# Performance work log

Hardware: AMD Instinct MI355X
Metric: run time of the kernel (lower is better)

## Reference

```python
import jax, jax.numpy as jnp
import numpy as np

K = 8  # leader_num
S = 8  # state_num


def setup_inputs() -> dict:
    key = jax.random.key(0)
    ks = jax.random.split(key, 11)
    B, L, C, H = 16, 720, 128, 96
    F2 = H // 2 + 1
    OUT = F2 * (2 * K + 1)
    return {
        "x": jax.random.normal(ks[0], (B, L, C), jnp.float32),
        "y_hat": jax.random.normal(ks[1], (B, H, C), jnp.float32),
        "temperature": jnp.ones((1,), jnp.float32),
        "cls_w": jax.random.normal(ks[2], (S, L), jnp.float32) * 0.02,
        "basic_state": jax.random.normal(ks[3], (C, S), jnp.float32) * 0.02,
        "state_bias": jax.random.normal(ks[4], (S,), jnp.float32) * 0.02,
        "mix_head_w": jax.random.normal(ks[5], (S, K * OUT), jnp.float32) * 0.05,
        "mix_head_b": jax.random.normal(ks[6], (S, OUT), jnp.float32) * 0.05,
        "mix_wr": jax.random.normal(ks[7], (F2, 3 * F2), jnp.float32) * 0.05,
        "mix_wi": jax.random.normal(ks[8], (F2, 3 * F2), jnp.float32) * 0.05,
        "mix_br": jax.random.normal(ks[9], (F2,), jnp.float32) * 0.05,
        "mix_bi": jax.random.normal(ks[10], (F2,), jnp.float32) * 0.05,
    }


def _leader_pipeline(xn, yn):
    # xn: [B,C,L] instance-normed lookback, yn: [B,C,H] normed forecast
    B, C, L = xn.shape
    H = yn.shape[-1]
    rf = jnp.fft.rfft(xn, axis=-1)  # [B,C,F]
    # full pairwise circular cross-correlation: [B,C,C,L]
    cc = jnp.fft.irfft(rf[:, :, None, :] * jnp.conj(rf)[:, None, :, :], n=L, axis=-1)
    ca = jnp.abs(cc)
    # local-max masking on interior points (drops first/last lag)
    mask = (ca[..., 1:-1] >= ca[..., :-2]) & (ca[..., 1:-1] >= ca[..., 2:])
    cc = cc[..., 1:-1] * mask / L  # [B,C,C,L-2]
    ca = jnp.abs(cc)
    shift = jnp.argmax(ca, axis=-1)  # [B,C,C] best lag per pair
    cmax = jnp.max(ca, axis=-1)
    _, leader_ids = jax.lax.top_k(cmax, K)  # [B,C,K]
    lead_corr = jnp.take_along_axis(cc, leader_ids[:, :, :, None], axis=2)  # [B,C,K,L-2]
    shift = jnp.take_along_axis(shift, leader_ids, axis=2)  # [B,C,K]
    r = jnp.take_along_axis(lead_corr, shift[..., None], axis=3)[..., 0]  # [B,C,K]
    shift = shift + 1  # account for the dropped first lag (local_max=True)
    # gather leader sequences and apply per-(sample,channel,leader) dynamic shift
    const_idx = jnp.arange(L, L + H)
    idx = const_idx[None, None, :] - shift.reshape(B, C * K, 1)  # [B,CK,H]
    seq = jnp.concatenate([xn, yn], -1)  # [B,C,L+H]
    seq = seq[jnp.arange(B)[:, None], leader_ids.reshape(B, C * K)]  # [B,CK,L+H]
    seq_shifted = jnp.take_along_axis(seq, idx, axis=-1).reshape(B, C, K, H)
    seq_shifted = seq_shifted * jnp.sign(r)[..., None]
    return seq_shifted, jnp.abs(r)


def reference(x, y_hat, temperature, cls_w, basic_state, state_bias,
              mix_head_w, mix_head_b, mix_wr, mix_wi, mix_br, mix_bi):
    B, L, C = x.shape
    H = y_hat.shape[1]
    F2 = H // 2 + 1
    xt = jnp.swapaxes(x, 1, 2)  # [B,C,L]
    yt = jnp.swapaxes(y_hat, 1, 2)  # [B,C,H]
    mu = xt.mean(-1, keepdims=True)
    xc = xt - mu
    std = jnp.sqrt((xc ** 2).mean(-1, keepdims=True) + 1e-8)
    xn = xc / std
    yn = (yt - mu) / std
    seq_shifted, r_abs = _leader_pipeline(xn, yn)  # torch.no_grad block
    seq_shifted = jax.lax.stop_gradient(seq_shifted)
    r_abs = jax.lax.stop_gradient(r_abs)
    ones = jnp.ones((B, C, 1), xt.dtype)
    rw = jax.nn.softmax(jnp.concatenate([ones, r_abs], -1) / temperature, axis=-1)
    corr_feat = rw[..., 1:]  # [B,C,K]
    # FilterFactory (num_state > 1, need_classifier): per-sample state mixture
    p = jax.nn.softmax(state_bias + basic_state + jnp.einsum('bcl,sl->bcs', xt, cls_w), axis=-1)  # [B,C,S]
    OUT = F2 * (2 * K + 1)
    w = jnp.einsum('bcs,sf->bcf', p, mix_head_w).reshape(B, C, K, OUT)
    b = jnp.einsum('bcs,so->bco', p, mix_head_b)
    filt = (jnp.einsum('bck,bcko->bco', corr_feat, w) + b).reshape(B, C, 2 * K + 1, F2)
    yf = jnp.fft.rfft(yn, axis=-1)  # [B,C,F2] complex64
    ssf = jnp.fft.rfft(seq_shifted, axis=-1) * filt[:, :, :K]  # [B,C,K,F2]
    sdf = (ssf - yf[:, :, None]) * filt[:, :, K:2 * K]
    yff = yf * filt[:, :, -1]
    catf = jnp.concatenate([ssf.sum(2), sdf.sum(2), yff], -1)  # [B,C,3*F2]
    mix_w = jax.lax.complex(mix_wr, mix_wi)  # [F2, 3*F2]
    mix_b = jax.lax.complex(mix_br, mix_bi)
    out_f = jnp.einsum('bcf,of->bco', catf, mix_w) + mix_b
    yn_new = yn + jnp.fft.irfft(out_f, n=H, axis=-1)
    y = yn_new * std + mu
    return jnp.swapaxes(y, 1, 2)  # [B,H,C]
```

## Files before the change

### kernel.cpp

```cpp
#include <hip/hip_runtime.h>
#include <math.h>

#define B_ 16
#define L_ 720
#define C_ 128
#define H_ 96
#define F2_ 49
#define K_ 8
#define S_ 8
#define OUT_ 833
#define SEQLEN 816
#define NF 361

__device__ __forceinline__ float2 cmulp(float2 a, float2 w) {
  return make_float2(a.x*w.x - a.y*w.y, a.x*w.y + a.y*w.x);
}

#define WSYNC() do { asm volatile("s_waitcnt lgkmcnt(0)" ::: "memory"); __builtin_amdgcn_sched_barrier(0); } while (0)

__device__ __constant__ float W5X[5] = {1.f, 0.30901699437494742f, -0.80901699437494745f, -0.80901699437494745f, 0.30901699437494742f};
__device__ __constant__ float W5Y[5] = {0.f, 0.95105651629515357f, 0.58778525229247312f, -0.58778525229247312f, -0.95105651629515357f};

__device__ __forceinline__ void dft8_pos(const float2 zin[8], float2 X[8]) {
  const float RH = 0.70710678118654752440f;
  const float2 A0 = make_float2(zin[0].x+zin[4].x, zin[0].y+zin[4].y);
  const float2 A1 = make_float2(zin[0].x-zin[4].x, zin[0].y-zin[4].y);
  const float2 A2 = make_float2(zin[2].x+zin[6].x, zin[2].y+zin[6].y);
  const float2 A3 = make_float2(zin[2].x-zin[6].x, zin[2].y-zin[6].y);
  const float2 A4 = make_float2(zin[1].x+zin[5].x, zin[1].y+zin[5].y);
  const float2 A5 = make_float2(zin[1].x-zin[5].x, zin[1].y-zin[5].y);
  const float2 A6 = make_float2(zin[3].x+zin[7].x, zin[3].y+zin[7].y);
  const float2 A7 = make_float2(zin[3].x-zin[7].x, zin[3].y-zin[7].y);
  const float2 B0 = make_float2(A0.x+A2.x, A0.y+A2.y);
  const float2 B1 = make_float2(A0.x-A2.x, A0.y-A2.y);
  const float2 B2 = make_float2(A4.x+A6.x, A4.y+A6.y);
  const float2 B3 = make_float2(A4.x-A6.x, A4.y-A6.y);
  X[0] = make_float2(B0.x+B2.x, B0.y+B2.y);
  X[4] = make_float2(B0.x-B2.x, B0.y-B2.y);
  X[2] = make_float2(B1.x - B3.y, B1.y + B3.x);
  X[6] = make_float2(B1.x + B3.y, B1.y - B3.x);
  const float2 CI   = make_float2(-A3.y, A3.x);
  const float2 W1s1 = make_float2((A5.x - A5.y)*RH, (A5.x + A5.y)*RH);
  const float2 W3s1 = make_float2((-A5.x - A5.y)*RH, (A5.x - A5.y)*RH);
  const float2 W1s3 = make_float2((A7.x - A7.y)*RH, (A7.x + A7.y)*RH);
  const float2 W3s3 = make_float2((-A7.x - A7.y)*RH, (A7.x - A7.y)*RH);
  X[1] = make_float2(A1.x + CI.x + W1s1.x + W3s3.x, A1.y + CI.y + W1s1.y + W3s3.y);
  X[5] = make_float2(A1.x + CI.x - W1s1.x - W3s3.x, A1.y + CI.y - W1s1.y - W3s3.y);
  X[3] = make_float2(A1.x - CI.x + W3s1.x + W1s3.x, A1.y - CI.y + W3s1.y + W1s3.y);
  X[7] = make_float2(A1.x - CI.x - W3s1.x - W1s3.x, A1.y - CI.y - W3s1.y - W1s3.y);
}

__global__ __launch_bounds__(256) void k0_tab(float2* __restrict__ wtab_g) {
  for (int k = threadIdx.x; k < L_; k += 256) {
    double ang = (double)k * 0.008726646259971647884;
    wtab_g[k] = make_float2((float)cos(ang), (float)sin(ang));
  }
}

__global__ __launch_bounds__(256) void k1_norm(const float* __restrict__ x,
                                               const float* __restrict__ yh,
                                               float* __restrict__ seq,
                                               float* __restrict__ mu_g,
                                               float* __restrict__ std_g) {
  const int bc = blockIdx.x;
  const int b = bc >> 7, c = bc & 127;
  const int tid = threadIdx.x;
  __shared__ float redA[4], redB[4];
  const float* xb = x + (size_t)b * L_ * C_ + c;

  float s = 0.f;
  for (int l = tid; l < L_; l += 256) s += xb[(size_t)l * C_];
  for (int off = 32; off; off >>= 1) s += __shfl_down(s, off, 64);
  if ((tid & 63) == 0) redA[tid >> 6] = s;
  __syncthreads();
  const float mu = (redA[0] + redA[1] + redA[2] + redA[3]) * (1.0f / L_);

  float vs = 0.f;
  for (int l = tid; l < L_; l += 256) { float d = xb[(size_t)l * C_] - mu; vs += d * d; }
  for (int off = 32; off; off >>= 1) vs += __shfl_down(vs, off, 64);
  if ((tid & 63) == 0) redB[tid >> 6] = vs;
  __syncthreads();
  const float stdv = sqrtf((redB[0] + redB[1] + redB[2] + redB[3]) * (1.0f / L_) + 1e-8f);
  const float inv = 1.0f / stdv;

  float* sq = seq + (size_t)bc * SEQLEN;
  for (int l = tid; l < L_; l += 256) sq[l] = (xb[(size_t)l * C_] - mu) * inv;
  const float* yb = yh + (size_t)b * H_ * C_ + c;
  for (int h = tid; h < H_; h += 256) sq[L_ + h] = (yb[(size_t)h * C_] - mu) * inv;
  if (tid == 0) { mu_g[bc] = mu; std_g[bc] = stdv; }
}

__global__ __launch_bounds__(256) void k1f_fwd(const float* __restrict__ seq,
                                               const float2* __restrict__ wtab_g,
                                               float2* __restrict__ Rc) {
  const int bc0 = blockIdx.x * 2;
  const int tid = threadIdx.x;
  __shared__ float xrow[2][L_];
  __shared__ float2 wt[L_];
  for (int k = tid; k < L_; k += 256) {
    wt[k] = wtab_g[k];
    xrow[0][k] = seq[(size_t)bc0 * SEQLEN + k];
    xrow[1][k] = seq[(size_t)(bc0 + 1) * SEQLEN + k];
  }
  __syncthreads();
  for (int u = tid; u < 2 * NF; u += 256) {
    const int row = u / NF, f = u - row * NF;
    float re = 0.f, im = 0.f;
    int m = 0;
    const float* xr = xrow[row];
    for (int l = 0; l < L_; ++l) {
      const float v = xr[l];
      const float2 w = wt[m];
      re = fmaf(v, w.x, re);
      im = fmaf(-v, w.y, im);
      m += f; if (m >= L_) m -= L_;
    }
    Rc[(size_t)(bc0 + row) * NF + f] = make_float2(re, im);
  }
}

__global__ __launch_bounds__(256, 2) void k2_fft(const float2* __restrict__ Rc,
                                                 const float2* __restrict__ wtab_g,
                                                 float* __restrict__ r_arr,
                                                 int* __restrict__ t_arr) {
  const int phys = blockIdx.x;
  int idx = (phys & 7) * 1152 + (phys >> 3);
  const int b = idx / 576;
  idx -= b * 576;
  int g = 0;
  while (true) { const int cnt = (8 - g) << 4; if (idx < cnt) break; idx -= cnt; ++g; }
  const int rows = 8 - g;
  const int c1 = (g << 4) + idx / rows;
  const int c2t = g + idx % rows;
  const int c2base = c2t << 4;
  const int tid = threadIdx.x;
  const int wid = tid >> 6, lane = tid & 63;

  __shared__ float2 r1c[NF];
  __shared__ float2 t9[81];
  __shared__ float2 t45[45];
  __shared__ float2 Yw[4][2][360];
  __shared__ __align__(16) float ccw[4][2][728];

  for (int f = tid; f < NF; f += 256) r1c[f] = Rc[((size_t)(b * C_ + c1)) * NF + f];
  for (int i = tid; i < 81; i += 256) { int a = i / 9, c = i % 9; t9[i] = wtab_g[80 * ((a * c) % 9)]; }
  for (int i = tid; i < 45; i += 256) { int bb = i / 9, c = i % 9; t45[i] = wtab_g[16 * bb * c]; }
  __syncthreads();

  const float SCALE = 1.0f / 518400.0f;

  for (int it = 0; it < 2; ++it) {
    const int c2A = c2base + (wid << 2) + 2 * it;
    if (c2A + 1 < c1) continue;
    const float2* R2A = Rc + ((size_t)(b * C_ + c2A)) * NF;
    const float2* R2B = R2A + NF;

    if (lane < 45) {
      const int K2 = lane;
      float2 zinA[8], zinB[8];
#pragma unroll
      for (int q1 = 0; q1 < 8; ++q1) {
        const int k = 45 * q1 + K2;
        const int fB = 360 - k;
        const float2 a1 = r1c[k];
        const float2 a2 = r1c[fB];
        const float2 w  = wtab_g[k];
        {
          const float2 b1 = R2A[k];
          const float2 b2 = R2A[fB];
          const float2 pA = make_float2(a1.x*b1.x + a1.y*b1.y, a1.y*b1.x - a1.x*b1.y);
          float2 pB = make_float2(a2.x*b2.x + a2.y*b2.y, a2.y*b2.x - a2.x*b2.y);
          pB.y = (k == 0) ? pB.y : -pB.y;
          const float2 E = make_float2(pA.x + pB.x, pA.y + pB.y);
          const float2 O = make_float2(pA.x - pB.x, pA.y - pB.y);
          const float2 Ow = cmulp(O, w);
          zinA[q1] = make_float2(E.x - Ow.y, E.y + Ow.x);
        }
        {
          const float2 b1 = R2B[k];
          const float2 b2 = R2B[fB];
          const float2 pA = make_float2(a1.x*b1.x + a1.y*b1.y, a1.y*b1.x - a1.x*b1.y);
          float2 pB = make_float2(a2.x*b2.x + a2.y*b2.y, a2.y*b2.x - a2.x*b2.y);
          pB.y = (k == 0) ? pB.y : -pB.y;
          const float2 E = make_float2(pA.x + pB.x, pA.y + pB.y);
          const float2 O = make_float2(pA.x - pB.x, pA.y - pB.y);
          const float2 Ow = cmulp(O, w);
          zinB[q1] = make_float2(E.x - Ow.y, E.y + Ow.x);
        }
      }
      float2 XA[8], XB[8];
      dft8_pos(zinA, XA);
      dft8_pos(zinB, XB);
      int m = 0;
#pragma unroll
      for (int n1 = 0; n1 < 8; ++n1) {
        const float2 w = wtab_g[m];
        Yw[wid][0][n1 * 45 + K2] = cmulp(XA[n1], w);
        Yw[wid][1][n1 * 45 + K2] = cmulp(XB[n1], w);
        m += 2 * K2;
      }
    }
    WSYNC();

    {
      const int n1 = lane >> 3;
      const int cq = lane & 7;
      const int nci = (cq == 0) ? 2 : 1;
      int cvals[2] = { cq, 8 };

      float2 T9r[2][9], T45r[2][5];
#pragma unroll
      for (int ci = 0; ci < 2; ++ci) if (ci < nci) {
        const int c = cvals[ci];
#pragma unroll
        for (int a = 0; a < 9; ++a) T9r[ci][a] = t9[9 * a + c];
#pragma unroll
        for (int bq = 0; bq < 5; ++bq) T45r[ci][bq] = t45[9 * bq + c];
      }

#pragma unroll
      for (int pp = 0; pp < 2; ++pp) {
        const float2* Yrow = &Yw[wid][pp][n1 * 45];
        float yr[2][5], yi[2][5];
#pragma unroll
        for (int ci = 0; ci < 2; ++ci)
#pragma unroll
          for (int d = 0; d < 5; ++d) { yr[ci][d] = 0.f; yi[ci][d] = 0.f; }

#pragma unroll
        for (int bq = 0; bq < 5; ++bq) {
          float2 z[9];
#pragma unroll
          for (int a = 0; a < 9; ++a) z[a] = Yrow[5 * a + bq];
#pragma unroll
          for (int ci = 0; ci < 2; ++ci) if (ci < nci) {
            float ur = 0.f, ui = 0.f;
#pragma unroll
            for (int a = 0; a < 9; ++a) {
              ur += z[a].x * T9r[ci][a].x - z[a].y * T9r[ci][a].y;
              ui += z[a].x * T9r[ci][a].y + z[a].y * T9r[ci][a].x;
            }
            const float2 tw = T45r[ci][bq];
            const float vr = ur * tw.x - ui * tw.y;
            const float vi = ur * tw.y + ui * tw.x;
#pragma unroll
            for (int d = 0; d < 5; ++d) {
              const int m = (bq * d) % 5;
              yr[ci][d] += vr * W5X[m] - vi * W5Y[m];
              yi[ci][d] += vr * W5Y[m] + vi * W5X[m];
            }
          }
        }
        float2* cc2 = (float2*)(&ccw[wid][pp][0]);
#pragma unroll
        for (int ci = 0; ci < 2; ++ci) if (ci < nci) {
          const int c = cvals[ci];
#pragma unroll
          for (int d = 0; d < 5; ++d) {
            const int n2 = c + 9 * d;
            cc2[n1 + 8 * n2] = make_float2(yr[ci][d], yi[ci][d]);
          }
        }
      }
    }
    WSYNC();

    {
      const int half = lane >> 5, sl = lane & 31;
      const int c2h = c2A + half;
      const float* cr = ccw[wid][half];
      float bvF = 0.f; int btF = 1;
      float bvM = 0.f; int uM  = 719;
      for (int i = sl; i < 719; i += 32) {
        const int u = i + 1;
        const float v  = fabsf(cr[u]);
        const float lf = fabsf(cr[u - 1]);
        const float rt = fabsf(cr[(u == 719) ? 0 : (u + 1)]);
        if (v >= lf && v >= rt) {
          if (u <= 718 && (v > bvF || (v == bvF && u < btF))) { bvF = v; btF = u; }
          if (u >= 2   && (v > bvM || (v == bvM && u > uM)))  { bvM = v; uM  = u; }
        }
      }
      for (int off = 16; off; off >>= 1) {
        const float ovF = __shfl_down(bvF, off, 32); const int otF = __shfl_down(btF, off, 32);
        if (ovF > bvF || (ovF == bvF && otF < btF)) { bvF = ovF; btF = otF; }
        const float ovM = __shfl_down(bvM, off, 32); const int ouM = __shfl_down(uM, off, 32);
        if (ovM > bvM || (ovM == bvM && ouM > uM)) { bvM = ovM; uM = ouM; }
      }
      if (sl == 0 && c2h >= c1) {
        const float rF = (bvF > 0.f) ? cr[btF] * SCALE : 0.f;
        const size_t o = ((size_t)(b * C_ + c1)) * C_ + c2h;
        r_arr[o] = rF; t_arr[o] = btF;
        if (c2h > c1) {
          const float rM = (bvM > 0.f) ? cr[uM] * SCALE : 0.f;
          const size_t o2 = ((size_t)(b * C_ + c2h)) * C_ + c1;
          r_arr[o2] = rM; t_arr[o2] = 720 - uM;
        }
      }
    }
    WSYNC();
  }
}

__global__ __launch_bounds__(256) void k3_leaders(const float* __restrict__ x,
                                                  const float* __restrict__ temperature,
                                                  const float* __restrict__ cls_w,
                                                  const float* __restrict__ basic_state,
                                                  const float* __restrict__ state_bias,
                                                  const float* __restrict__ mhw,
                                                  const float* __restrict__ mhb,
                                                  const float* __restrict__ r_arr,
                                                  const int* __restrict__ t_arr,
                                                  int* __restrict__ lead_id,
                                                  int* __restrict__ lead_t,
                                                  float* __restrict__ lead_sr,
                                                  float* __restrict__ filt) {
  const int bc = blockIdx.x;
  const int b = bc >> 7, c = bc & 127;
  const int tid = threadIdx.x;
  __shared__ float caL[C_], rL[C_];
  __shared__ int tL[C_];
  __shared__ float xrowL[L_];
  __shared__ float cfL[K_], srL[K_], pL[S_], qL[S_ * K_], praw[S_];
  __shared__ int leadL[K_], ltL[K_];

  const float* xb = x + (size_t)b * L_ * C_ + c;
  for (int l = tid; l < L_; l += 256) xrowL[l] = xb[(size_t)l * C_];
  if (tid < C_) {
    const float r = r_arr[(size_t)bc * C_ + tid];
    rL[tid] = r; caL[tid] = fabsf(r);
    tL[tid] = t_arr[(size_t)bc * C_ + tid];
  }
  __syncthreads();

  if (tid == 0) {
    const float T = temperature[0];
    float lg[K_ + 1];
    lg[0] = 1.0f / T;
    for (int k = 0; k < K_; ++k) {
      float bvv = -1.f; int bi = 0;
      for (int jj = 0; jj < C_; ++jj) { const float v = caL[jj]; if (v > bvv) { bvv = v; bi = jj; } }
      leadL[k] = bi; ltL[k] = tL[bi];
      const float rv = rL[bi];
      srL[k] = (rv > 0.f) ? 1.f : ((rv < 0.f) ? -1.f : 0.f);
      lg[k + 1] = bvv / T;
      caL[bi] = -2.f;
    }
    float m = lg[0];
    for (int k = 1; k <= K_; ++k) m = fmaxf(m, lg[k]);
    float sum = 0.f, e[K_ + 1];
    for (int k = 0; k <= K_; ++k) { e[k] = expf(lg[k] - m); sum += e[k]; }
    const float invs = 1.0f / sum;
    for (int k = 0; k < K_; ++k) cfL[k] = e[k + 1] * invs;
  }
  __syncthreads();

  {
    const int gg = tid >> 5, lane = tid & 31;
    float acc = 0.f;
    const float* w = cls_w + (size_t)gg * L_;
    for (int l = lane; l < L_; l += 32) acc += xrowL[l] * w[l];
    for (int off = 16; off; off >>= 1) acc += __shfl_down(acc, off, 32);
    if (lane == 0) praw[gg] = acc + state_bias[gg] + basic_state[c * S_ + gg];
  }
  __syncthreads();
  if (tid == 0) {
    float m = praw[0];
    for (int s2 = 1; s2 < S_; ++s2) m = fmaxf(m, praw[s2]);
    float sum = 0.f;
    for (int s2 = 0; s2 < S_; ++s2) { const float e = expf(praw[s2] - m); pL[s2] = e; sum += e; }
    const float invs = 1.0f / sum;
    for (int s2 = 0; s2 < S_; ++s2) pL[s2] *= invs;
    for (int s2 = 0; s2 < S_; ++s2)
      for (int k = 0; k < K_; ++k) qL[s2 * K_ + k] = pL[s2] * cfL[k];
  }
  __syncthreads();

  for (int o = tid; o < OUT_; o += 256) {
    float acc = 0.f;
#pragma unroll
    for (int s2 = 0; s2 < S_; ++s2) {
      acc += pL[s2] * mhb[s2 * OUT_ + o];
#pragma unroll
      for (int k = 0; k < K_; ++k)
        acc += qL[s2 * K_ + k] * mhw[(size_t)s2 * (K_ * OUT_) + k * OUT_ + o];
    }
    filt[(size_t)bc * OUT_ + o] = acc;
  }
  if (tid < K_) {
    lead_id[bc * K_ + tid] = leadL[tid];
    lead_t[bc * K_ + tid] = ltL[tid];
    lead_sr[bc * K_ + tid] = srL[tid];
  }
}

__global__ __launch_bounds__(256) void k4_final(const float* __restrict__ seq,
                                                const float* __restrict__ mu_g,
                                                const float* __restrict__ std_g,
                                                const int* __restrict__ lead_id,
                                                const int* __restrict__ lead_t,
                                                const float* __restrict__ lead_sr,
                                                const float* __restrict__ filt,
                                                const float* __restrict__ mwr,
                                                const float* __restrict__ mwi,
                                                const float* __restrict__ mbr,
                                                const float* __restrict__ mbi,
                                                float* __restrict__ out) {
  const int bc = blockIdx.x;
  const int b = bc >> 7, c = bc & 127;
  const int tid = threadIdx.x;
  __shared__ float cosT[96], sinT[96];
  __shared__ float ssL[K_][H_], ynL[H_], flL[OUT_];
  __shared__ float sfr[K_][F2_], sfi[K_][F2_], yfr[F2_], yfi[F2_];
  __shared__ float catr[3 * F2_], cati[3 * F2_], ofr[F2_], ofi[F2_];
  __shared__ int ldL[K_], ltL[K_];
  __shared__ float srL[K_];

  if (tid < 96) {
    const float ang = (float)tid * (float)(6.283185307179586 / 96.0);
    cosT[tid] = cosf(ang); sinT[tid] = sinf(ang);
    ynL[tid] = seq[(size_t)bc * SEQLEN + L_ + tid];
  }
  if (tid >= 96 && tid < 96 + K_) {
    const int k = tid - 96;
    ldL[k] = lead_id[bc * K_ + k];
    ltL[k] = lead_t[bc * K_ + k];
    srL[k] = lead_sr[bc * K_ + k];
  }
  for (int o = tid; o < OUT_; o += 256) flL[o] = filt[(size_t)bc * OUT_ + o];
  __syncthreads();

  for (int i = tid; i < K_ * H_; i += 256) {
    const int k = i / H_, h = i - k * H_;
    ssL[k][h] = seq[((size_t)(b * C_ + ldL[k])) * SEQLEN + (L_ + h - ltL[k])] * srL[k];
  }
  __syncthreads();

  for (int u = tid; u < K_ * F2_ + F2_; u += 256) {
    if (u < K_ * F2_) {
      const int k = u / F2_, f = u - k * F2_;
      float re = 0.f, im = 0.f; int m = 0;
      for (int h = 0; h < H_; ++h) {
        const float v = ssL[k][h];
        re = fmaf(v, cosT[m], re); im = fmaf(-v, sinT[m], im);
        m += f; if (m >= 96) m -= 96;
      }
      sfr[k][f] = re; sfi[k][f] = im;
    } else {
      const int f = u - K_ * F2_;
      float re = 0.f, im = 0.f; int m = 0;
      for (int h = 0; h < H_; ++h) {
        const float v = ynL[h];
        re = fmaf(v, cosT[m], re); im = fmaf(-v, sinT[m], im);
        m += f; if (m >= 96) m -= 96;
      }
      yfr[f] = re; yfi[f] = im;
    }
  }
  __syncthreads();

  if (tid < F2_) {
    const int f = tid;
    float s1r = 0.f, s1i = 0.f, s2r = 0.f, s2i = 0.f;
    const float yr = yfr[f], yi = yfi[f];
#pragma unroll
    for (int k = 0; k < K_; ++k) {
      const float fa = flL[k * F2_ + f], fb = flL[(K_ + k) * F2_ + f];
      const float ar = sfr[k][f] * fa, ai = sfi[k][f] * fa;
      s1r += ar; s1i += ai;
      s2r += (ar - yr) * fb; s2i += (ai - yi) * fb;
    }
    const float fc = flL[2 * K_ * F2_ + f];
    catr[f] = s1r;            cati[f] = s1i;
    catr[F2_ + f] = s2r;      cati[F2_ + f] = s2i;
    catr[2 * F2_ + f] = yr * fc; cati[2 * F2_ + f] = yi * fc;
  }
  __syncthreads();

  if (tid < F2_) {
    const int o = tid;
    float ar = mbr[o], ai = mbi[o];
    const float* wr = mwr + (size_t)o * (3 * F2_);
    const float* wi = mwi + (size_t)o * (3 * F2_);
    for (int f = 0; f < 3 * F2_; ++f) {
      const float cr = catr[f], ci = cati[f];
      const float wrr = wr[f], wii = wi[f];
      ar += cr * wrr - ci * wii;
      ai += cr * wii + ci * wrr;
    }
    ofr[o] = ar; ofi[o] = ai;
  }
  __syncthreads();

  if (tid < H_) {
    const int h = tid;
    float val = ofr[0] + ofr[48] * ((h & 1) ? -1.f : 1.f);
    int m = h;
    for (int f = 1; f < 48; ++f) {
      val += 2.f * (ofr[f] * cosT[m] - ofi[f] * sinT[m]);
      m += h; if (m >= 96) m -= 96;
    }
    val *= (1.0f / 96.0f);
    const float mu = mu_g[bc], stdv = std_g[bc];
    out[((size_t)b * H_ + h) * C_ + c] = (ynL[h] + val) * stdv + mu;
  }
}

extern "C" void kernel_launch(void* const* d_in, const int* in_sizes, int n_in,
                              void* d_out, int out_size, void* d_ws, size_t ws_size,
                              hipStream_t stream) {
  const float* x    = (const float*)d_in[0];
  const float* yh   = (const float*)d_in[1];
  const float* temp = (const float*)d_in[2];
  const float* clsw = (const float*)d_in[3];
  const float* bst  = (const float*)d_in[4];
  const float* sbias= (const float*)d_in[5];
  const float* mhw  = (const float*)d_in[6];
  const float* mhb  = (const float*)d_in[7];
  const float* mwr  = (const float*)d_in[8];
  const float* mwi  = (const float*)d_in[9];
  const float* mbr  = (const float*)d_in[10];
  const float* mbi  = (const float*)d_in[11];
  float* out = (float*)d_out;

  float* ws = (float*)d_ws;
  float* seq    = ws;
  float* mu_g   = seq + (size_t)2048 * SEQLEN;
  float* std_g  = mu_g + 2048;
  float* r_arr  = std_g + 2048;
  float* filt   = r_arr + (size_t)2048 * C_;
  int*   t_arr  = (int*)(filt + (size_t)2048 * OUT_);
  int*   lead_i = t_arr + (size_t)2048 * C_;
  int*   lead_t = lead_i + 2048 * K_;
  float* lead_s = (float*)(lead_t + 2048 * K_);
  float2* wtab  = (float2*)(lead_s + 2048 * K_);

  float2* Rc = (float2*)filt;

  hipLaunchKernelGGL(k0_tab, dim3(1), dim3(256), 0, stream, wtab);
  hipLaunchKernelGGL(k1_norm, dim3(B_ * C_), dim3(256), 0, stream, x, yh, seq, mu_g, std_g);
  hipLaunchKernelGGL(k1f_fwd, dim3(B_ * C_ / 2), dim3(256), 0, stream, seq, wtab, Rc);
  hipLaunchKernelGGL(k2_fft, dim3(B_ * 576), dim3(256), 0, stream, Rc, wtab, r_arr, t_arr);
  hipLaunchKernelGGL(k3_leaders, dim3(B_ * C_), dim3(256), 0, stream,
                     x, temp, clsw, bst, sbias, mhw, mhb, r_arr, t_arr,
                     lead_i, lead_t, lead_s, filt);
  hipLaunchKernelGGL(k4_final, dim3(B_ * C_), dim3(256), 0, stream,
                     seq, mu_g, std_g, lead_i, lead_t, lead_s, filt,
                     mwr, mwi, mbr, mbi, out);
}
```

Baseline: 867.3 us.

## Fuse normalization into forward DFT, merge leader and final kernels, rebalance FFT lanes

The normalization kernel is folded into the forward DFT kernel: each block loads two adjacent channels with float2 loads, computes mean and std in shared memory, and transforms the rows in place, so seq is no longer re-read. The leader-selection and final filter/mix kernels are merged into one block per (b,c), which keeps the filter, leader ids, shifts and scales in shared memory and drops their global round-trip and one launch. In k2_fft the two-pair work per lane is split over 90 lanes in two passes instead of 45 lanes doing both pairs, lowering per-thread register pressure. The merged kernel uses more shared memory per block, which may reduce occupancy, and one __syncthreads was removed.

```diff
diff --git a/kernel.cpp b/kernel.cpp
--- a/kernel.cpp
+++ b/kernel.cpp
@@ -57,52 +57,57 @@
   }
 }
 
-__global__ __launch_bounds__(256) void k1_norm(const float* __restrict__ x,
-                                               const float* __restrict__ yh,
-                                               float* __restrict__ seq,
-                                               float* __restrict__ mu_g,
-                                               float* __restrict__ std_g) {
-  const int bc = blockIdx.x;
-  const int b = bc >> 7, c = bc & 127;
-  const int tid = threadIdx.x;
-  __shared__ float redA[4], redB[4];
-  const float* xb = x + (size_t)b * L_ * C_ + c;
-
-  float s = 0.f;
-  for (int l = tid; l < L_; l += 256) s += xb[(size_t)l * C_];
-  for (int off = 32; off; off >>= 1) s += __shfl_down(s, off, 64);
-  if ((tid & 63) == 0) redA[tid >> 6] = s;
-  __syncthreads();
-  const float mu = (redA[0] + redA[1] + redA[2] + redA[3]) * (1.0f / L_);
-
-  float vs = 0.f;
-  for (int l = tid; l < L_; l += 256) { float d = xb[(size_t)l * C_] - mu; vs += d * d; }
-  for (int off = 32; off; off >>= 1) vs += __shfl_down(vs, off, 64);
-  if ((tid & 63) == 0) redB[tid >> 6] = vs;
-  __syncthreads();
-  const float stdv = sqrtf((redB[0] + redB[1] + redB[2] + redB[3]) * (1.0f / L_) + 1e-8f);
-  const float inv = 1.0f / stdv;
-
-  float* sq = seq + (size_t)bc * SEQLEN;
-  for (int l = tid; l < L_; l += 256) sq[l] = (xb[(size_t)l * C_] - mu) * inv;
-  const float* yb = yh + (size_t)b * H_ * C_ + c;
-  for (int h = tid; h < H_; h += 256) sq[L_ + h] = (yb[(size_t)h * C_] - mu) * inv;
-  if (tid == 0) { mu_g[bc] = mu; std_g[bc] = stdv; }
-}
-
-__global__ __launch_bounds__(256) void k1f_fwd(const float* __restrict__ seq,
-                                               const float2* __restrict__ wtab_g,
-                                               float2* __restrict__ Rc) {
+__global__ __launch_bounds__(256) void k1_fused(const float* __restrict__ x,
+                                                const float* __restrict__ yh,
+                                                const float2* __restrict__ wtab_g,
+                                                float* __restrict__ seq,
+                                                float* __restrict__ mu_g,
+                                                float* __restrict__ std_g,
+                                                float2* __restrict__ Rc) {
   const int bc0 = blockIdx.x * 2;
+  const int b = bc0 >> 7, c0 = bc0 & 127;
   const int tid = threadIdx.x;
   __shared__ float xrow[2][L_];
+  __shared__ float yrow[2][H_];
   __shared__ float2 wt[L_];
-  for (int k = tid; k < L_; k += 256) {
-    wt[k] = wtab_g[k];
-    xrow[0][k] = seq[(size_t)bc0 * SEQLEN + k];
-    xrow[1][k] = seq[(size_t)(bc0 + 1) * SEQLEN + k];
-  }
-  __syncthreads();
+  __shared__ float red[4];
+
+  const float* xb = x + (size_t)b * L_ * C_ + c0;
+  for (int l = tid; l < L_; l += 256) {
+    const float2 v = *(const float2*)&xb[(size_t)l * C_];
+    xrow[0][l] = v.x; xrow[1][l] = v.y;
+  }
+  const float* yb = yh + (size_t)b * H_ * C_ + c0;
+  if (tid < H_) {
+    const float2 v = *(const float2*)&yb[(size_t)tid * C_];
+    yrow[0][tid] = v.x; yrow[1][tid] = v.y;
+  }
+  for (int k = tid; k < L_; k += 256) wt[k] = wtab_g[k];
+  __syncthreads();
+
+  for (int ch = 0; ch < 2; ++ch) {
+    float s = 0.f;
+    for (int l = tid; l < L_; l += 256) s += xrow[ch][l];
+    for (int off = 32; off; off >>= 1) s += __shfl_down(s, off, 64);
+    if ((tid & 63) == 0) red[tid >> 6] = s;
+    __syncthreads();
+    const float mu = (red[0] + red[1] + red[2] + red[3]) * (1.0f / L_);
+    __syncthreads();
+    float vs = 0.f;
+    for (int l = tid; l < L_; l += 256) { float d = xrow[ch][l] - mu; vs += d * d; }
+    for (int off = 32; off; off >>= 1) vs += __shfl_down(vs, off, 64);
+    if ((tid & 63) == 0) red[tid >> 6] = vs;
+    __syncthreads();
+    const float stdv = sqrtf((red[0] + red[1] + red[2] + red[3]) * (1.0f / L_) + 1e-8f);
+    const float inv = 1.0f / stdv;
+    if (tid == 0) { mu_g[bc0 + ch] = mu; std_g[bc0 + ch] = stdv; }
+    __syncthreads();
+    float* sq = seq + (size_t)(bc0 + ch) * SEQLEN;
+    for (int l = tid; l < L_; l += 256) { const float v = (xrow[ch][l] - mu) * inv; xrow[ch][l] = v; sq[l] = v; }
+    if (tid < H_) sq[L_ + tid] = (yrow[ch][tid] - mu) * inv;
+    __syncthreads();
+  }
+
   for (int u = tid; u < 2 * NF; u += 256) {
     const int row = u / NF, f = u - row * NF;
     float re = 0.f, im = 0.f;
@@ -155,49 +160,39 @@
     const float2* R2A = Rc + ((size_t)(b * C_ + c2A)) * NF;
     const float2* R2B = R2A + NF;
 
-    if (lane < 45) {
-      const int K2 = lane;
-      float2 zinA[8], zinB[8];
-#pragma unroll
-      for (int q1 = 0; q1 < 8; ++q1) {
-        const int k = 45 * q1 + K2;
-        const int fB = 360 - k;
-        const float2 a1 = r1c[k];
-        const float2 a2 = r1c[fB];
-        const float2 w  = wtab_g[k];
-        {
-          const float2 b1 = R2A[k];
-          const float2 b2 = R2A[fB];
+#pragma unroll
+    for (int pass = 0; pass < 2; ++pass) {
+      const int t = lane + (pass << 6);
+      if (t < 90) {
+        const int pr = (t >= 45) ? 1 : 0;
+        const int K2 = t - 45 * pr;
+        const float2* R2 = pr ? R2B : R2A;
+        float2 zin[8];
+#pragma unroll
+        for (int q1 = 0; q1 < 8; ++q1) {
+          const int k = 45 * q1 + K2;
+          const int fB = 360 - k;
+          const float2 a1 = r1c[k];
+          const float2 a2 = r1c[fB];
+          const float2 w  = wtab_g[k];
+          const float2 b1 = R2[k];
+          const float2 b2 = R2[fB];
           const float2 pA = make_float2(a1.x*b1.x + a1.y*b1.y, a1.y*b1.x - a1.x*b1.y);
           float2 pB = make_float2(a2.x*b2.x + a2.y*b2.y, a2.y*b2.x - a2.x*b2.y);
           pB.y = (k == 0) ? pB.y : -pB.y;
           const float2 E = make_float2(pA.x + pB.x, pA.y + pB.y);
           const float2 O = make_float2(pA.x - pB.x, pA.y - pB.y);
           const float2 Ow = cmulp(O, w);
-          zinA[q1] = make_float2(E.x - Ow.y, E.y + Ow.x);
+          zin[q1] = make_float2(E.x - Ow.y, E.y + Ow.x);
         }
-        {
-          const float2 b1 = R2B[k];
-          const float2 b2 = R2B[fB];
-          const float2 pA = make_float2(a1.x*b1.x + a1.y*b1.y, a1.y*b1.x - a1.x*b1.y);
-          float2 pB = make_float2(a2.x*b2.x + a2.y*b2.y, a2.y*b2.x - a2.x*b2.y);
-          pB.y = (k == 0) ? pB.y : -pB.y;
-          const float2 E = make_float2(pA.x + pB.x, pA.y + pB.y);
-          const float2 O = make_float2(pA.x - pB.x, pA.y - pB.y);
-          const float2 Ow = cmulp(O, w);
-          zinB[q1] = make_float2(E.x - Ow.y, E.y + Ow.x);
+        float2 X[8];
+        dft8_pos(zin, X);
+        int m = 0;
+#pragma unroll
+        for (int n1 = 0; n1 < 8; ++n1) {
+          Yw[wid][pr][n1 * 45 + K2] = cmulp(X[n1], wtab_g[m]);
+          m += 2 * K2;
         }
-      }
-      float2 XA[8], XB[8];
-      dft8_pos(zinA, XA);
-      dft8_pos(zinB, XB);
-      int m = 0;
-#pragma unroll
-      for (int n1 = 0; n1 < 8; ++n1) {
-        const float2 w = wtab_g[m];
-        Yw[wid][0][n1 * 45 + K2] = cmulp(XA[n1], w);
-        Yw[wid][1][n1 * 45 + K2] = cmulp(XB[n1], w);
-        m += 2 * K2;
       }
     }
     WSYNC();
@@ -302,19 +297,23 @@
   }
 }
 
-__global__ __launch_bounds__(256) void k3_leaders(const float* __restrict__ x,
-                                                  const float* __restrict__ temperature,
-                                                  const float* __restrict__ cls_w,
-                                                  const float* __restrict__ basic_state,
-                                                  const float* __restrict__ state_bias,
-                                                  const float* __restrict__ mhw,
-                                                  const float* __restrict__ mhb,
-                                                  const float* __restrict__ r_arr,
-                                                  const int* __restrict__ t_arr,
-                                                  int* __restrict__ lead_id,
-                                                  int* __restrict__ lead_t,
-                                                  float* __restrict__ lead_sr,
-                                                  float* __restrict__ filt) {
+__global__ __launch_bounds__(256) void k34_fused(const float* __restrict__ x,
+                                                 const float* __restrict__ temperature,
+                                                 const float* __restrict__ cls_w,
+                                                 const float* __restrict__ basic_state,
+                                                 const float* __restrict__ state_bias,
+                                                 const float* __restrict__ mhw,
+                                                 const float* __restrict__ mhb,
+                                                 const float* __restrict__ r_arr,
+                                                 const int* __restrict__ t_arr,
+                                                 const float* __restrict__ seq,
+                                                 const float* __restrict__ mu_g,
+                                                 const float* __restrict__ std_g,
+                                                 const float* __restrict__ mwr,
+                                                 const float* __restrict__ mwi,
+                                                 const float* __restrict__ mbr,
+                                                 const float* __restrict__ mbi,
+                                                 float* __restrict__ out) {
   const int bc = blockIdx.x;
   const int b = bc >> 7, c = bc & 127;
   const int tid = threadIdx.x;
@@ -323,6 +322,10 @@
   __shared__ float xrowL[L_];
   __shared__ float cfL[K_], srL[K_], pL[S_], qL[S_ * K_], praw[S_];
   __shared__ int leadL[K_], ltL[K_];
+  __shared__ float cosT[96], sinT[96];
+  __shared__ float ssL[K_][H_], ynL[H_], flL[OUT_];
+  __shared__ float sfr[K_][F2_], sfi[K_][F2_], yfr[F2_], yfi[F2_];
+  __shared__ float catr[3 * F2_], cati[3 * F2_], ofr[F2_], ofi[F2_];
 
   const float* xb = x + (size_t)b * L_ * C_ + c;
   for (int l = tid; l < L_; l += 256) xrowL[l] = xb[(size_t)l * C_];
@@ -330,6 +333,12 @@
     const float r = r_arr[(size_t)bc * C_ + tid];
     rL[tid] = r; caL[tid] = fabsf(r);
     tL[tid] = t_arr[(size_t)bc * C_ + tid];
+  }
+  if (tid >= 128 && tid < 224) {
+    const int h = tid - 128;
+    const float ang = (float)h * (float)(6.283185307179586 / 96.0);
+    cosT[h] = cosf(ang); sinT[h] = sinf(ang);
+    ynL[h] = seq[(size_t)bc * SEQLEN + L_ + h];
   }
   __syncthreads();
 
@@ -353,7 +362,6 @@
     const float invs = 1.0f / sum;
     for (int k = 0; k < K_; ++k) cfL[k] = e[k + 1] * invs;
   }
-  __syncthreads();
 
   {
     const int gg = tid >> 5, lane = tid & 31;
@@ -385,54 +393,11 @@
       for (int k = 0; k < K_; ++k)
         acc += qL[s2 * K_ + k] * mhw[(size_t)s2 * (K_ * OUT_) + k * OUT_ + o];
     }
-    filt[(size_t)bc * OUT_ + o] = acc;
-  }
-  if (tid < K_) {
-    lead_id[bc * K_ + tid] = leadL[tid];
-    lead_t[bc * K_ + tid] = ltL[tid];
-    lead_sr[bc * K_ + tid] = srL[tid];
-  }
-}
-
-__global__ __launch_bounds__(256) void k4_final(const float* __restrict__ seq,
-                                                const float* __restrict__ mu_g,
-                                                const float* __restrict__ std_g,
-                                                const int* __restrict__ lead_id,
-                                                const int* __restrict__ lead_t,
-                                                const float* __restrict__ lead_sr,
-                                                const float* __restrict__ filt,
-                                                const float* __restrict__ mwr,
-                                                const float* __restrict__ mwi,
-                                                const float* __restrict__ mbr,
-                                                const float* __restrict__ mbi,
-                                                float* __restrict__ out) {
-  const int bc = blockIdx.x;
-  const int b = bc >> 7, c = bc & 127;
-  const int tid = threadIdx.x;
-  __shared__ float cosT[96], sinT[96];
-  __shared__ float ssL[K_][H_], ynL[H_], flL[OUT_];
-  __shared__ float sfr[K_][F2_], sfi[K_][F2_], yfr[F2_], yfi[F2_];
-  __shared__ float catr[3 * F2_], cati[3 * F2_], ofr[F2_], ofi[F2_];
-  __shared__ int ldL[K_], ltL[K_];
-  __shared__ float srL[K_];
-
-  if (tid < 96) {
-    const float ang = (float)tid * (float)(6.283185307179586 / 96.0);
-    cosT[tid] = cosf(ang); sinT[tid] = sinf(ang);
-    ynL[tid] = seq[(size_t)bc * SEQLEN + L_ + tid];
-  }
-  if (tid >= 96 && tid < 96 + K_) {
-    const int k = tid - 96;
-    ldL[k] = lead_id[bc * K_ + k];
-    ltL[k] = lead_t[bc * K_ + k];
-    srL[k] = lead_sr[bc * K_ + k];
-  }
-  for (int o = tid; o < OUT_; o += 256) flL[o] = filt[(size_t)bc * OUT_ + o];
-  __syncthreads();
-
+    flL[o] = acc;
+  }
   for (int i = tid; i < K_ * H_; i += 256) {
     const int k = i / H_, h = i - k * H_;
-    ssL[k][h] = seq[((size_t)(b * C_ + ldL[k])) * SEQLEN + (L_ + h - ltL[k])] * srL[k];
+    ssL[k][h] = seq[((size_t)(b * C_ + leadL[k])) * SEQLEN + (L_ + h - ltL[k])] * srL[k];
   }
   __syncthreads();
 
@@ -528,23 +493,14 @@
   float* mu_g   = seq + (size_t)2048 * SEQLEN;
   float* std_g  = mu_g + 2048;
   float* r_arr  = std_g + 2048;
-  float* filt   = r_arr + (size_t)2048 * C_;
-  int*   t_arr  = (int*)(filt + (size_t)2048 * OUT_);
-  int*   lead_i = t_arr + (size_t)2048 * C_;
-  int*   lead_t = lead_i + 2048 * K_;
-  float* lead_s = (float*)(lead_t + 2048 * K_);
-  float2* wtab  = (float2*)(lead_s + 2048 * K_);
-
-  float2* Rc = (float2*)filt;
+  int*   t_arr  = (int*)(r_arr + (size_t)2048 * C_);
+  float2* Rc    = (float2*)(t_arr + (size_t)2048 * C_);
+  float2* wtab  = Rc + (size_t)2048 * NF;
 
   hipLaunchKernelGGL(k0_tab, dim3(1), dim3(256), 0, stream, wtab);
-  hipLaunchKernelGGL(k1_norm, dim3(B_ * C_), dim3(256), 0, stream, x, yh, seq, mu_g, std_g);
-  hipLaunchKernelGGL(k1f_fwd, dim3(B_ * C_ / 2), dim3(256), 0, stream, seq, wtab, Rc);
+  hipLaunchKernelGGL(k1_fused, dim3(B_ * C_ / 2), dim3(256), 0, stream, x, yh, wtab, seq, mu_g, std_g, Rc);
   hipLaunchKernelGGL(k2_fft, dim3(B_ * 576), dim3(256), 0, stream, Rc, wtab, r_arr, t_arr);
-  hipLaunchKernelGGL(k3_leaders, dim3(B_ * C_), dim3(256), 0, stream,
+  hipLaunchKernelGGL(k34_fused, dim3(B_ * C_), dim3(256), 0, stream,
                      x, temp, clsw, bst, sbias, mhw, mhb, r_arr, t_arr,
-                     lead_i, lead_t, lead_s, filt);
-  hipLaunchKernelGGL(k4_final, dim3(B_ * C_), dim3(256), 0, stream,
-                     seq, mu_g, std_g, lead_i, lead_t, lead_s, filt,
-                     mwr, mwi, mbr, mbi, out);
-}
+                     seq, mu_g, std_g, mwr, mwi, mbr, mbi, out);
+}
```

Measured after the change: 947.9 us. 9.3% more time.
